# Performance work log

Hardware: AMD Instinct MI355X
Metric: run time of the kernel (lower is better)

Reference implementation:

```python
import jax, jax.numpy as jnp
import numpy as np

N_TOKENS = 16384
HIDDEN = 1024
FFN = 4 * HIDDEN
N_EXPERTS = 8
TOP_K = 2


def setup_inputs() -> dict:
    key = jax.random.key(0)
    ks = jax.random.split(key, 7)
    s = 0.02
    return {
        "x": jax.random.normal(ks[0], (N_TOKENS, HIDDEN), jnp.float32),
        "Wg": jax.random.normal(ks[1], (HIDDEN, N_EXPERTS), jnp.float32) * s,
        "bg": jnp.zeros((N_EXPERTS,), jnp.float32),
        "W1": jax.random.normal(ks[2], (N_EXPERTS, HIDDEN, FFN), jnp.float32) * s,
        "b1": jnp.zeros((N_EXPERTS, FFN), jnp.float32),
        "W2": jax.random.normal(ks[3], (N_EXPERTS, FFN, HIDDEN), jnp.float32) * s,
        "b2": jnp.zeros((N_EXPERTS, HIDDEN), jnp.float32),
    }


def reference(x, Wg, bg, W1, b1, W2, b2):
    # Gate + top-k routing (softmax over the k selected logits, as in the torch code)
    gate_scores = x @ Wg + bg                              # [N, E]
    topk_scores, topk_idx = jax.lax.top_k(gate_scores, TOP_K)  # [N, k]
    topk_w = jax.nn.softmax(topk_scores, axis=1)           # [N, k]

    n, e = gate_scores.shape
    # Dense per-(token, expert) combine weights; zero for non-selected experts.
    w_dense = jnp.zeros((n, e), x.dtype).at[
        jnp.arange(n)[:, None], topk_idx
    ].add(topk_w)                                          # [N, E]

    # Loop over the small fixed expert set; tokens fully vectorized per expert.
    out = jnp.zeros_like(x)
    for ei in range(e):
        h = jax.nn.relu(x @ W1[ei] + b1[ei])               # [N, FFN]
        y = h @ W2[ei] + b2[ei]                            # [N, H]
        out = out + y * w_dense[:, ei:ei + 1]
    return out
```

## Files before the change

### kernel.cpp

```cpp
#include <hip/hip_runtime.h>
#include <stdint.h>

#define N_TOKENS 16384
#define HIDDEN   1024
#define FFN      4096
#define N_EXPERTS 8
#define NBLK     (N_TOKENS / 256)
#define MAX_TILES 264
#define MAX_ROWS (MAX_TILES * 128)
#define NB_HALF  2048

typedef __attribute__((ext_vector_type(8))) short short8;
typedef __attribute__((ext_vector_type(4))) float f32x4;

__device__ inline unsigned short f2bf(float f) {
  union { float f; unsigned u; } c; c.f = f;
  unsigned u = c.u;
  unsigned r = (u + 0x7fffu + ((u >> 16) & 1u)) >> 16;
  return (unsigned short)r;
}

__device__ inline void gld_lds16(const unsigned short* g, unsigned short* l) {
  __builtin_amdgcn_global_load_lds(
      (const __attribute__((address_space(1))) void*)g,
      (__attribute__((address_space(3))) void*)l, 16, 0, 0);
}


__global__ __launch_bounds__(256) void gate_kernel(
    const float* __restrict__ x, const float* __restrict__ Wg,
    const float* __restrict__ bg, int* __restrict__ gate_idx,
    float* __restrict__ gate_w)
{
  int lane = threadIdx.x & 63;
  int wv = threadIdx.x >> 6;
  int t = blockIdx.x * 4 + wv;
  const float* xr = x + (size_t)t * HIDDEN;
  float acc[N_EXPERTS];
#pragma unroll
  for (int e = 0; e < N_EXPERTS; e++) acc[e] = 0.f;
#pragma unroll
  for (int i = 0; i < HIDDEN / 64; i++) {
    int h = i * 64 + lane;
    float xv = xr[h];
    const float4* wv4 = (const float4*)(Wg + (size_t)h * N_EXPERTS);
    float4 w01 = wv4[0], w23 = wv4[1];
    acc[0] = fmaf(xv, w01.x, acc[0]); acc[1] = fmaf(xv, w01.y, acc[1]);
    acc[2] = fmaf(xv, w01.z, acc[2]); acc[3] = fmaf(xv, w01.w, acc[3]);
    acc[4] = fmaf(xv, w23.x, acc[4]); acc[5] = fmaf(xv, w23.y, acc[5]);
    acc[6] = fmaf(xv, w23.z, acc[6]); acc[7] = fmaf(xv, w23.w, acc[7]);
  }
#pragma unroll
  for (int off = 32; off > 0; off >>= 1)
#pragma unroll
    for (int e = 0; e < N_EXPERTS; e++)
      acc[e] += __shfl_down(acc[e], off, 64);
  if (lane == 0) {
    float s[N_EXPERTS];
#pragma unroll
    for (int e = 0; e < N_EXPERTS; e++) s[e] = acc[e] + bg[e];
    int e0 = 0;
#pragma unroll
    for (int e = 1; e < N_EXPERTS; e++) if (s[e] > s[e0]) e0 = e;
    int e1 = (e0 == 0) ? 1 : 0;
#pragma unroll
    for (int e = 0; e < N_EXPERTS; e++) if (e != e0 && s[e] > s[e1]) e1 = e;
    float d = s[e1] - s[e0];
    float ex = __expf(d);
    float w0 = 1.f / (1.f + ex);
    float w1 = ex / (1.f + ex);
    gate_idx[2 * t] = e0; gate_idx[2 * t + 1] = e1;
    gate_w[2 * t] = w0;  gate_w[2 * t + 1] = w1;
  }
}

__global__ __launch_bounds__(256) void count_kernel(
    const int* __restrict__ gate_idx, int* __restrict__ blockCounts)
{
  __shared__ int h[N_EXPERTS];
  if (threadIdx.x < N_EXPERTS) h[threadIdx.x] = 0;
  __syncthreads();
  int t = blockIdx.x * 256 + threadIdx.x;
  atomicAdd(&h[gate_idx[2 * t]], 1);
  atomicAdd(&h[gate_idx[2 * t + 1]], 1);
  __syncthreads();
  if (threadIdx.x < N_EXPERTS)
    blockCounts[blockIdx.x * N_EXPERTS + threadIdx.x] = h[threadIdx.x];
}

__global__ void scan_kernel(const int* __restrict__ blockCounts,
                            int* __restrict__ blockBase, int* __restrict__ meta)
{
  __shared__ int totals[N_EXPERTS];
  __shared__ int offs[N_EXPERTS + 1];
  int e = threadIdx.x;
  if (e < N_EXPERTS) {
    int run = 0;
    for (int b = 0; b < NBLK; b++) {
      blockBase[b * N_EXPERTS + e] = run;
      run += blockCounts[b * N_EXPERTS + e];
    }
    totals[e] = run;
  }
  __syncthreads();
  if (threadIdx.x == 0) {
    int off = 0;
    for (int ee = 0; ee < N_EXPERTS; ee++) {
      offs[ee] = off;
      meta[16 + ee] = off;
      off += ((totals[ee] + 127) >> 7) << 7;
    }
    offs[N_EXPERTS] = off;
    meta[16 + N_EXPERTS] = off;
    int ntiles = off >> 7;
    meta[25] = ntiles;
    int ee = 0;
    for (int t = 0; t < ntiles; t++) {
      while (offs[ee + 1] <= (t << 7)) ee++;
      meta[32 + t] = ee;
    }
  }
  __syncthreads();
  if (e < N_EXPERTS) {
    int o = offs[e];
    for (int b = 0; b < NBLK; b++)
      blockBase[b * N_EXPERTS + e] += o;
  }
}

__global__ __launch_bounds__(256) void place_kernel(
    const int* __restrict__ gate_idx, const float* __restrict__ gate_w,
    const int* __restrict__ blockBase, int* __restrict__ pair_token,
    float* __restrict__ pair_w)
{
  __shared__ int cur[N_EXPERTS];
  if (threadIdx.x < N_EXPERTS)
    cur[threadIdx.x] = blockBase[blockIdx.x * N_EXPERTS + threadIdx.x];
  __syncthreads();
  int t = blockIdx.x * 256 + threadIdx.x;
#pragma unroll
  for (int k = 0; k < 2; k++) {
    int e = gate_idx[2 * t + k];
    int pos = atomicAdd(&cur[e], 1);
    pair_token[pos] = t;
    pair_w[pos] = gate_w[2 * t + k];
  }
}

__global__ __launch_bounds__(256) void gather_kernel(
    const float* __restrict__ x, const int* __restrict__ pair_token,
    unsigned short* __restrict__ Xg)
{
  int r = blockIdx.x;
  int t = pair_token[r];
  if (t < 0) return;
  const float4* src = (const float4*)(x + (size_t)t * HIDDEN);
  float4 v = src[threadIdx.x];
  ushort4 o;
  o.x = f2bf(v.x); o.y = f2bf(v.y); o.z = f2bf(v.z); o.w = f2bf(v.w);
  ((ushort4*)(Xg + (size_t)r * HIDDEN))[threadIdx.x] = o;
}

__global__ __launch_bounds__(256) void transpose_bf16_kernel(
    const float* __restrict__ in, unsigned short* __restrict__ out, int R, int C)
{
  __shared__ float tile[64][65];
  int e = blockIdx.z;
  int r0 = blockIdx.y * 64, c0 = blockIdx.x * 64;
  int tr = threadIdx.x >> 4, tc = threadIdx.x & 15;
  const float* src = in + ((size_t)e * R + r0) * C + c0;
#pragma unroll
  for (int rr = 0; rr < 4; rr++) {
    int row = rr * 16 + tr;
    float4 v = *(const float4*)(src + (size_t)row * C + tc * 4);
    tile[row][tc * 4 + 0] = v.x; tile[row][tc * 4 + 1] = v.y;
    tile[row][tc * 4 + 2] = v.z; tile[row][tc * 4 + 3] = v.w;
  }
  __syncthreads();
  unsigned short* dst = out + ((size_t)e * C + c0) * R + r0;
#pragma unroll
  for (int rr = 0; rr < 4; rr++) {
    int crow = rr * 16 + tr;
    ushort4 o;
    o.x = f2bf(tile[tc * 4 + 0][crow]);
    o.y = f2bf(tile[tc * 4 + 1][crow]);
    o.z = f2bf(tile[tc * 4 + 2][crow]);
    o.w = f2bf(tile[tc * 4 + 3][crow]);
    *(ushort4*)(dst + (size_t)crow * R + tc * 4) = o;
  }
}

template<int EPI>
__global__ __launch_bounds__(256, 4) void moe_gemm_kernel(
    const unsigned short* __restrict__ A,
    const unsigned short* __restrict__ Bt,
    const float* __restrict__ bias,
    unsigned short* __restrict__ Hout,
    float* __restrict__ out,
    const int* __restrict__ meta,
    const int* __restrict__ pair_token,
    const float* __restrict__ pair_w,
    int lda, int ldb, int bkoff, int klen, int nbase, int nbfull)
{
  int ntiles = meta[25];

  int gx = gridDim.x;
  int nwg = gx * gridDim.y;
  int lid = blockIdx.y * gx + blockIdx.x;
  int q = nwg >> 3, r8 = nwg & 7;
  int xcd = lid & 7, pos = lid >> 3;
  int aid = (xcd < r8 ? xcd * (q + 1) : r8 * (q + 1) + (xcd - r8) * q) + pos;
  int rt = aid / gx;
  int ct = aid % gx;
  if (rt >= ntiles) return;
  int row0 = rt << 7;
  int e = meta[32 + rt];

  __shared__ __align__(16) unsigned short As[128 * 64];
  __shared__ __align__(16) unsigned short Bs[128 * 64];

  int tid = threadIdx.x;
  int lane = tid & 63, wv = tid >> 6;
  int wm = wv >> 1, wn = wv & 1;
  int quad = lane >> 4, l16 = lane & 15, l7 = l16 & 7;

  int r0c = tid >> 3;
  int csw = ((tid & 7) ^ (r0c & 7)) << 3;
  const unsigned short* gA = A + (size_t)(row0 + r0c) * lda + csw;
  const unsigned short* gB = Bt + ((size_t)e * nbfull + nbase + (ct << 7) + r0c) * ldb
                             + bkoff + csw;
  unsigned short* lA = As + tid * 8;
  unsigned short* lB = Bs + tid * 8;

  auto STAGE = [&](int k0) {
#pragma unroll
    for (int k = 0; k < 4; k++) {
      gld_lds16(gA + (size_t)(32 * k) * lda + k0, lA + k * 2048);
      gld_lds16(gB + (size_t)(32 * k) * ldb + k0, lB + k * 2048);
    }
  };

  int ca0 = (quad ^ l7) << 3;
  int ca1 = ((4 + quad) ^ l7) << 3;
  int abase = (wm * 64 + l16) * 64;
  int bbase = (wn * 64 + l16) * 64;

  f32x4 acc[4][4];
  f32x4 zero = {0.f, 0.f, 0.f, 0.f};
#pragma unroll
  for (int i = 0; i < 4; i++)
#pragma unroll
    for (int j = 0; j < 4; j++) acc[i][j] = zero;

  int NT = klen >> 6;

  STAGE(0);
  for (int t = 0; t < NT; t++) {
    __syncthreads();
    {
      short8 a[4], b[4];
#pragma unroll
      for (int mf = 0; mf < 4; mf++)
        a[mf] = *(const short8*)(As + abase + mf * 1024 + ca0);
#pragma unroll
      for (int nf = 0; nf < 4; nf++)
        b[nf] = *(const short8*)(Bs + bbase + nf * 1024 + ca0);
#pragma unroll
      for (int mf = 0; mf < 4; mf++)
#pragma unroll
        for (int nf = 0; nf < 4; nf++)
          acc[mf][nf] = __builtin_amdgcn_mfma_f32_16x16x32_bf16(
              a[mf], b[nf], acc[mf][nf], 0, 0, 0);
    }
    {
      short8 a[4], b[4];
#pragma unroll
      for (int mf = 0; mf < 4; mf++)
        a[mf] = *(const short8*)(As + abase + mf * 1024 + ca1);
#pragma unroll
      for (int nf = 0; nf < 4; nf++)
        b[nf] = *(const short8*)(Bs + bbase + nf * 1024 + ca1);
#pragma unroll
      for (int mf = 0; mf < 4; mf++)
#pragma unroll
        for (int nf = 0; nf < 4; nf++)
          acc[mf][nf] = __builtin_amdgcn_mfma_f32_16x16x32_bf16(
              a[mf], b[nf], acc[mf][nf], 0, 0, 0);
    }
    __syncthreads();
    if (t + 1 < NT) STAGE((t + 1) << 6);
  }

  if (EPI == 0) {
#pragma unroll
    for (int mf = 0; mf < 4; mf++) {
      size_t hr = (size_t)row0 + wm * 64 + mf * 16 + quad * 4;
#pragma unroll
      for (int nf = 0; nf < 4; nf++) {
        int hcol = (ct << 7) + wn * 64 + nf * 16 + l16;
        float bb = bias[(size_t)e * nbfull + nbase + hcol];
#pragma unroll
        for (int j = 0; j < 4; j++) {
          float v = fmaxf(acc[mf][nf][j] + bb, 0.f);
          Hout[(hr + j) * (size_t)NB_HALF + hcol] = f2bf(v);
        }
      }
    }
  } else {
#pragma unroll
    for (int mf = 0; mf < 4; mf++) {
      int rbase = row0 + wm * 64 + mf * 16 + quad * 4;
      int tok[4]; float wgt[4];
#pragma unroll
      for (int j = 0; j < 4; j++) {
        tok[j] = pair_token[rbase + j];
        wgt[j] = pair_w[rbase + j];
      }
#pragma unroll
      for (int nf = 0; nf < 4; nf++) {
        int gcol = (ct << 7) + wn * 64 + nf * 16 + l16;
        float bb = bias ? bias[(size_t)e * nbfull + gcol] : 0.f;
#pragma unroll
        for (int j = 0; j < 4; j++) {
          if (tok[j] >= 0)
            atomicAdd(out + (size_t)tok[j] * HIDDEN + gcol,
                      wgt[j] * (acc[mf][nf][j] + bb));
        }
      }
    }
  }
}

extern "C" void kernel_launch(void* const* d_in, const int* in_sizes, int n_in,
                              void* d_out, int out_size, void* d_ws, size_t ws_size,
                              hipStream_t stream)
{
  const float* x  = (const float*)d_in[0];
  const float* Wg = (const float*)d_in[1];
  const float* bg = (const float*)d_in[2];
  const float* W1 = (const float*)d_in[3];
  const float* b1 = (const float*)d_in[4];
  const float* W2 = (const float*)d_in[5];
  const float* b2 = (const float*)d_in[6];
  float* out = (float*)d_out;

  char* ws = (char*)d_ws;
  size_t off = 0;
  auto alloc = [&](size_t bytes) {
    char* p = ws + off;
    off += (bytes + 255) & ~(size_t)255;
    return p;
  };
  int* gate_idx          = (int*)alloc((size_t)N_TOKENS * 2 * sizeof(int));
  float* gate_w          = (float*)alloc((size_t)N_TOKENS * 2 * sizeof(float));
  int* meta              = (int*)alloc(2048);
  int* blockCounts       = (int*)alloc((size_t)NBLK * N_EXPERTS * sizeof(int));
  int* blockBase         = (int*)alloc((size_t)NBLK * N_EXPERTS * sizeof(int));
  int* pair_token        = (int*)alloc((size_t)MAX_ROWS * sizeof(int));
  float* pair_w          = (float*)alloc((size_t)MAX_ROWS * sizeof(float));
  unsigned short* Xg     = (unsigned short*)alloc((size_t)MAX_ROWS * HIDDEN * 2);
  unsigned short* W1T    = (unsigned short*)alloc((size_t)N_EXPERTS * FFN * HIDDEN * 2);
  unsigned short* W2T    = (unsigned short*)alloc((size_t)N_EXPERTS * HIDDEN * FFN * 2);
  unsigned short* H      = (unsigned short*)alloc((size_t)MAX_ROWS * NB_HALF * 2);

  hipMemsetAsync(pair_token, 0xFF, (size_t)MAX_ROWS * sizeof(int), stream);
  hipMemsetAsync(out, 0, (size_t)N_TOKENS * HIDDEN * sizeof(float), stream);

  gate_kernel<<<N_TOKENS / 4, 256, 0, stream>>>(x, Wg, bg, gate_idx, gate_w);
  count_kernel<<<NBLK, 256, 0, stream>>>(gate_idx, blockCounts);
  scan_kernel<<<1, 64, 0, stream>>>(blockCounts, blockBase, meta);
  place_kernel<<<NBLK, 256, 0, stream>>>(gate_idx, gate_w, blockBase,
                                         pair_token, pair_w);
  gather_kernel<<<MAX_ROWS, 256, 0, stream>>>(x, pair_token, Xg);
  transpose_bf16_kernel<<<dim3(FFN / 64, HIDDEN / 64, N_EXPERTS), 256, 0, stream>>>(
      W1, W1T, HIDDEN, FFN);
  transpose_bf16_kernel<<<dim3(HIDDEN / 64, FFN / 64, N_EXPERTS), 256, 0, stream>>>(
      W2, W2T, FFN, HIDDEN);

  for (int fh = 0; fh < 2; fh++) {
    int nb = fh * NB_HALF;
    moe_gemm_kernel<0><<<dim3(NB_HALF / 128, MAX_TILES), 256, 0, stream>>>(
        Xg, W1T, b1, H, nullptr, meta, nullptr, nullptr,
        HIDDEN, HIDDEN, 0, HIDDEN, nb, FFN);
    moe_gemm_kernel<1><<<dim3(HIDDEN / 128, MAX_TILES), 256, 0, stream>>>(
        H, W2T, fh == 0 ? b2 : nullptr, nullptr, out, meta, pair_token, pair_w,
        NB_HALF, FFN, nb, NB_HALF, 0, HIDDEN);
  }
}
```

Baseline: 1.239 ms.

## Use 512-thread workgroups with 2x4 wave grid in MoE GEMM

Doubles the workgroup to 8 waves for the same 128x128 output tile. Each wave now computes 64x32 instead of 64x64, which halves the accumulator registers, and each thread issues half as many global-to-LDS loads per stage. The aim is more waves per CU to hide load and barrier latency. In exchange, each wave reuses its A fragments over fewer MFMAs, so LDS read traffic per MFMA goes up, and barriers must now synchronise 8 waves.

Result: faster. 1.190 ms (-3.9%).

```diff
diff --git a/kernel.cpp b/kernel.cpp
--- a/kernel.cpp
+++ b/kernel.cpp
@@ -191,7 +191,7 @@
 }
 
 template<int EPI>
-__global__ __launch_bounds__(256, 4) void moe_gemm_kernel(
+__global__ __launch_bounds__(512, 6) void moe_gemm_kernel(
     const unsigned short* __restrict__ A,
     const unsigned short* __restrict__ Bt,
     const float* __restrict__ bias,
@@ -221,7 +221,7 @@
 
   int tid = threadIdx.x;
   int lane = tid & 63, wv = tid >> 6;
-  int wm = wv >> 1, wn = wv & 1;
+  int wm = wv >> 2, wn = wv & 3;
   int quad = lane >> 4, l16 = lane & 15, l7 = l16 & 7;
 
   int r0c = tid >> 3;
@@ -233,60 +233,46 @@
   unsigned short* lB = Bs + tid * 8;
 
   auto STAGE = [&](int k0) {
-#pragma unroll
-    for (int k = 0; k < 4; k++) {
-      gld_lds16(gA + (size_t)(32 * k) * lda + k0, lA + k * 2048);
-      gld_lds16(gB + (size_t)(32 * k) * ldb + k0, lB + k * 2048);
-    }
+    gld_lds16(gA + k0, lA);
+    gld_lds16(gA + (size_t)64 * lda + k0, lA + 4096);
+    gld_lds16(gB + k0, lB);
+    gld_lds16(gB + (size_t)64 * ldb + k0, lB + 4096);
   };
 
   int ca0 = (quad ^ l7) << 3;
   int ca1 = ((4 + quad) ^ l7) << 3;
   int abase = (wm * 64 + l16) * 64;
-  int bbase = (wn * 64 + l16) * 64;
-
-  f32x4 acc[4][4];
+  int bbase = (wn * 32 + l16) * 64;
+
+  f32x4 acc[4][2];
   f32x4 zero = {0.f, 0.f, 0.f, 0.f};
 #pragma unroll
   for (int i = 0; i < 4; i++)
 #pragma unroll
-    for (int j = 0; j < 4; j++) acc[i][j] = zero;
+    for (int j = 0; j < 2; j++) acc[i][j] = zero;
 
   int NT = klen >> 6;
 
   STAGE(0);
   for (int t = 0; t < NT; t++) {
     __syncthreads();
-    {
-      short8 a[4], b[4];
+#pragma unroll
+    for (int h = 0; h < 2; h++) {
+      int ca = h ? ca1 : ca0;
+      short8 a[4], b[2];
+#pragma unroll
+      for (int nf = 0; nf < 2; nf++)
+        b[nf] = *(const short8*)(Bs + bbase + nf * 1024 + ca);
 #pragma unroll
       for (int mf = 0; mf < 4; mf++)
-        a[mf] = *(const short8*)(As + abase + mf * 1024 + ca0);
-#pragma unroll
-      for (int nf = 0; nf < 4; nf++)
-        b[nf] = *(const short8*)(Bs + bbase + nf * 1024 + ca0);
+        a[mf] = *(const short8*)(As + abase + mf * 1024 + ca);
 #pragma unroll
       for (int mf = 0; mf < 4; mf++)
 #pragma unroll
-        for (int nf = 0; nf < 4; nf++)
+        for (int nf = 0; nf < 2; nf++)
           acc[mf][nf] = __builtin_amdgcn_mfma_f32_16x16x32_bf16(
               a[mf], b[nf], acc[mf][nf], 0, 0, 0);
     }
-    {
-      short8 a[4], b[4];
-#pragma unroll
-      for (int mf = 0; mf < 4; mf++)
-        a[mf] = *(const short8*)(As + abase + mf * 1024 + ca1);
-#pragma unroll
-      for (int nf = 0; nf < 4; nf++)
-        b[nf] = *(const short8*)(Bs + bbase + nf * 1024 + ca1);
-#pragma unroll
-      for (int mf = 0; mf < 4; mf++)
-#pragma unroll
-        for (int nf = 0; nf < 4; nf++)
-          acc[mf][nf] = __builtin_amdgcn_mfma_f32_16x16x32_bf16(
-              a[mf], b[nf], acc[mf][nf], 0, 0, 0);
-    }
     __syncthreads();
     if (t + 1 < NT) STAGE((t + 1) << 6);
   }
@@ -296,8 +282,8 @@
     for (int mf = 0; mf < 4; mf++) {
       size_t hr = (size_t)row0 + wm * 64 + mf * 16 + quad * 4;
 #pragma unroll
-      for (int nf = 0; nf < 4; nf++) {
-        int hcol = (ct << 7) + wn * 64 + nf * 16 + l16;
+      for (int nf = 0; nf < 2; nf++) {
+        int hcol = (ct << 7) + wn * 32 + nf * 16 + l16;
         float bb = bias[(size_t)e * nbfull + nbase + hcol];
 #pragma unroll
         for (int j = 0; j < 4; j++) {
@@ -317,8 +303,8 @@
         wgt[j] = pair_w[rbase + j];
       }
 #pragma unroll
-      for (int nf = 0; nf < 4; nf++) {
-        int gcol = (ct << 7) + wn * 64 + nf * 16 + l16;
+      for (int nf = 0; nf < 2; nf++) {
+        int gcol = (ct << 7) + wn * 32 + nf * 16 + l16;
         float bb = bias ? bias[(size_t)e * nbfull + gcol] : 0.f;
 #pragma unroll
         for (int j = 0; j < 4; j++) {
@@ -379,10 +365,10 @@
 
   for (int fh = 0; fh < 2; fh++) {
     int nb = fh * NB_HALF;
-    moe_gemm_kernel<0><<<dim3(NB_HALF / 128, MAX_TILES), 256, 0, stream>>>(
+    moe_gemm_kernel<0><<<dim3(NB_HALF / 128, MAX_TILES), 512, 0, stream>>>(
         Xg, W1T, b1, H, nullptr, meta, nullptr, nullptr,
         HIDDEN, HIDDEN, 0, HIDDEN, nb, FFN);
-    moe_gemm_kernel<1><<<dim3(HIDDEN / 128, MAX_TILES), 256, 0, stream>>>(
+    moe_gemm_kernel<1><<<dim3(HIDDEN / 128, MAX_TILES), 512, 0, stream>>>(
         H, W2T, fh == 0 ? b2 : nullptr, nullptr, out, meta, pair_token, pair_w,
         NB_HALF, FFN, nb, NB_HALF, 0, HIDDEN);
   }
```
